# Performance work log

Hardware: AMD Instinct MI355X
Metric: run time of the kernel (lower is better)

The kernel has to match this reference:

```python
import jax, jax.numpy as jnp
import numpy as np

TOPK = 13
NC = 80
ALPHA = 1.0
BETA = 6.0
EPS = 1e-9
TN = 256
IMG = 640


def _make_anchor_points():
    # standard YOLO anchor centers for strides 8,16,32 on a 640x640 image -> 8400 points
    pts = []
    for s in (8, 16, 32):
        n = IMG // s
        xs = (np.arange(n, dtype=np.float32) + 0.5) * s
        gx, gy = np.meshgrid(xs, xs)
        pts.append(np.stack([gx.ravel(), gy.ravel()], axis=-1))
    return jnp.asarray(np.concatenate(pts, axis=0))  # (8400, 2)


def setup_inputs() -> dict:
    key = jax.random.key(0)
    k1, k2, k3, k4, k5, k6 = jax.random.split(key, 6)
    anc_points = _make_anchor_points()
    grids = anc_points.shape[0]
    pd_scores = jax.random.uniform(k1, (TN, grids, NC), dtype=jnp.float32)
    # predicted boxes: valid xyxy around random centers
    pc = jax.random.uniform(k2, (TN, grids, 2), dtype=jnp.float32) * IMG
    pwh = jax.random.uniform(k3, (TN, grids, 2), dtype=jnp.float32) * 64.0 + 4.0
    pd_bboxes = jnp.concatenate([pc - pwh * 0.5, pc + pwh * 0.5], axis=-1)
    gc = jax.random.uniform(k4, (TN, 2), dtype=jnp.float32) * IMG
    gwh = jax.random.uniform(k5, (TN, 2), dtype=jnp.float32) * 160.0 + 16.0
    gt_bboxes = jnp.concatenate([gc - gwh * 0.5, gc + gwh * 0.5], axis=-1)
    gt_labels = jax.random.randint(k6, (TN, 1), 0, NC, dtype=jnp.int32)
    return {"pd_scores": pd_scores, "pd_bboxes": pd_bboxes, "anc_points": anc_points,
            "gt_labels": gt_labels, "gt_bboxes": gt_bboxes}


def _iou(box1, box2):
    # box1: (tn,4) xyxy, box2: (tn,grids,4) xyxy -> (tn,grids)
    b1 = box1[:, None, :]
    x1y1 = jnp.maximum(b1[..., 0:2], box2[..., 0:2])
    x2y2 = jnp.minimum(b1[..., 2:4], box2[..., 2:4])
    overlap = jnp.clip(x2y2 - x1y1, 0).prod(-1)
    area1 = jnp.clip(b1[..., 2:4] - b1[..., 0:2], 0).prod(-1)
    area2 = jnp.clip(box2[..., 2:4] - box2[..., 0:2], 0).prod(-1)
    return overlap / (area1 + area2 - overlap + EPS)


def _candidates_in_gts(xy_centers, gt_bboxes):
    # xy_centers: (grids,2), gt_bboxes: (tn,4) -> (tn,grids) float {0,1}
    lt = xy_centers[None, :, :] - gt_bboxes[:, None, 0:2]   # (tn,grids,2)
    rb = gt_bboxes[:, None, 2:4] - xy_centers[None, :, :]   # (tn,grids,2)
    deltas = jnp.concatenate([lt, rb], axis=-1)             # (tn,grids,4)
    return (deltas.min(axis=-1) > EPS).astype(gt_bboxes.dtype)


def _topk_mask(metrics):
    # metrics: (tn,grids) -> binary mask of per-row top-k entries
    tn, grids = metrics.shape
    _, idxs = jax.lax.top_k(metrics, TOPK)                  # (tn,TOPK)
    rows = jnp.arange(tn)[:, None]
    return jnp.zeros((tn, grids), metrics.dtype).at[rows, idxs].add(1.0)


def reference(pd_scores, pd_bboxes, anc_points, gt_labels, gt_bboxes):
    tn, grids, nc = pd_scores.shape
    gt_lab = gt_labels.astype(jnp.int32)                    # (tn,1)
    # per-target class score at its gt label: (tn,grids)
    idx = jnp.broadcast_to(gt_lab[:, :, None], (tn, grids, 1))
    bbox_scores = jnp.take_along_axis(pd_scores, idx, axis=2).squeeze(-1)
    overlaps = _iou(gt_bboxes, pd_bboxes)                   # (tn,grids)
    align_metric = (bbox_scores ** ALPHA) * (overlaps ** BETA)
    mask_in_gts = _candidates_in_gts(anc_points, gt_bboxes)
    mask_topk = _topk_mask(align_metric * mask_in_gts)
    mask_pos = mask_topk * mask_in_gts                      # (tn,grids)
    # targets
    target_labels = jnp.where(mask_pos == 1, gt_lab, 0).astype(jnp.int32)  # (tn,grids)
    target_bboxes = jnp.where(mask_pos[..., None] == 1, gt_bboxes[:, None, :], 0.0)
    onehot = jax.nn.one_hot(target_labels, NC, dtype=pd_scores.dtype)
    target_scores = jnp.where(mask_pos[..., None] > 0, onehot, 0.0)
    # normalization of scores by aligned metric
    am = align_metric * mask_pos
    pos_align = am.max(axis=-1, keepdims=True)
    pos_overlaps = (overlaps * mask_pos).max(axis=-1, keepdims=True)
    norm = (am * pos_overlaps / (pos_align + EPS))[..., None]
    target_scores = target_scores * norm
    return target_labels, target_bboxes, target_scores, mask_pos.astype(bool)
```

## Files before the change

### kernel.cpp

```cpp
#include <hip/hip_runtime.h>

#define GRIDS 8400
#define TNB   256
#define NCV   80
#define TOPKV 13
#define EPSF  1e-9f

__global__ __launch_bounds__(256) void taa_kernel(
    const float* __restrict__ pd_scores,
    const float* __restrict__ pd_bboxes,
    const float* __restrict__ anc,
    const int*   __restrict__ gt_labels,
    const float* __restrict__ gt_bboxes,
    float* __restrict__ out_labels,
    float* __restrict__ out_bboxes,
    float* __restrict__ out_scores,
    float* __restrict__ out_mask)
{
    __shared__ float smet[GRIDS];
    __shared__ float rv[256];
    __shared__ int   ri[256];
    __shared__ int   sel_idx[TOPKV];
    __shared__ float sel_val[TOPKV];
    __shared__ float sel_am[TOPKV];
    __shared__ float sel_ov[TOPKV];
    __shared__ int   sel_in[TOPKV];

    const int t   = blockIdx.x;
    const int tid = threadIdx.x;

    const float gx1 = gt_bboxes[t*4+0];
    const float gy1 = gt_bboxes[t*4+1];
    const float gx2 = gt_bboxes[t*4+2];
    const float gy2 = gt_bboxes[t*4+3];
    const int   lab = gt_labels[t];
    const float garea = fmaxf(gx2-gx1, 0.f) * fmaxf(gy2-gy1, 0.f);

    const float4* pb = reinterpret_cast<const float4*>(pd_bboxes) + (size_t)t*GRIDS;
    const float*  ps = pd_scores + (size_t)t*GRIDS*NCV + lab;

    for (int g = tid; g < GRIDS; g += 256) {
        float ax = anc[2*g], ay = anc[2*g+1];
        float dmin = fminf(fminf(ax-gx1, ay-gy1), fminf(gx2-ax, gy2-ay));
        float4 p = pb[g];
        float ix1 = fmaxf(gx1, p.x), iy1 = fmaxf(gy1, p.y);
        float ix2 = fminf(gx2, p.z), iy2 = fminf(gy2, p.w);
        float ov  = fmaxf(ix2-ix1, 0.f) * fmaxf(iy2-iy1, 0.f);
        float pa  = fmaxf(p.z-p.x, 0.f) * fmaxf(p.w-p.y, 0.f);
        float iou = ov / (garea + pa - ov + EPSF);
        float sc  = ps[(size_t)g*NCV];
        float i2  = iou*iou;
        float m   = sc * (i2*i2*i2);
        smet[g] = (dmin > EPSF) ? m : 0.f;
    }
    __syncthreads();

    for (int k = 0; k < TOPKV; ++k) {
        float bv = -1.f; int bi = GRIDS;
        for (int g = tid; g < GRIDS; g += 256) {
            float v = smet[g];
            if (v > bv) { bv = v; bi = g; }
        }
        rv[tid] = bv; ri[tid] = bi;
        __syncthreads();
        for (int s = 128; s > 0; s >>= 1) {
            if (tid < s) {
                float v2 = rv[tid+s]; int j2 = ri[tid+s];
                if (v2 > rv[tid] || (v2 == rv[tid] && j2 < ri[tid])) { rv[tid] = v2; ri[tid] = j2; }
            }
            __syncthreads();
        }
        if (tid == 0) {
            int gi = ri[0];
            sel_idx[k] = gi;
            sel_val[k] = rv[0];
            smet[gi] = -1.f;
        }
        __syncthreads();
    }

    if (tid < TOPKV) {
        int g = sel_idx[tid];
        float ax = anc[2*g], ay = anc[2*g+1];
        float dmin = fminf(fminf(ax-gx1, ay-gy1), fminf(gx2-ax, gy2-ay));
        bool ing = dmin > EPSF;
        float4 p = pb[g];
        float ix1 = fmaxf(gx1, p.x), iy1 = fmaxf(gy1, p.y);
        float ix2 = fminf(gx2, p.z), iy2 = fminf(gy2, p.w);
        float ov  = fmaxf(ix2-ix1, 0.f) * fmaxf(iy2-iy1, 0.f);
        float pa  = fmaxf(p.z-p.x, 0.f) * fmaxf(p.w-p.y, 0.f);
        float iou = ov / (garea + pa - ov + EPSF);
        sel_in[tid] = ing ? 1 : 0;
        sel_am[tid] = ing ? sel_val[tid] : 0.f;
        sel_ov[tid] = ing ? iou : 0.f;
    }
    __syncthreads();

    if (tid < TOPKV && sel_in[tid]) {
        float pa = 0.f, po = 0.f;
        for (int k = 0; k < TOPKV; ++k) {
            pa = fmaxf(pa, sel_am[k]);
            po = fmaxf(po, sel_ov[k]);
        }
        float norm = sel_am[tid] * po / (pa + EPSF);
        int g = sel_idx[tid];
        size_t off = (size_t)t*GRIDS + g;
        out_labels[off] = (float)lab;
        out_mask[off]   = 1.0f;
        float4 gb; gb.x = gx1; gb.y = gy1; gb.z = gx2; gb.w = gy2;
        reinterpret_cast<float4*>(out_bboxes)[off] = gb;
        out_scores[off*(size_t)NCV + lab] = norm;
    }
}

extern "C" void kernel_launch(void* const* d_in, const int* in_sizes, int n_in,
                              void* d_out, int out_size, void* d_ws, size_t ws_size,
                              hipStream_t stream)
{
    const float* pd_scores = (const float*)d_in[0];
    const float* pd_bboxes = (const float*)d_in[1];
    const float* anc       = (const float*)d_in[2];
    const int*   gt_labels = (const int*)d_in[3];
    const float* gt_bboxes = (const float*)d_in[4];
    float* out = (float*)d_out;

    hipMemsetAsync(d_out, 0, (size_t)out_size * sizeof(float), stream);

    float* out_labels = out;
    float* out_bboxes = out_labels + (size_t)TNB*GRIDS;
    float* out_scores = out_bboxes + (size_t)TNB*GRIDS*4;
    float* out_mask   = out_scores + (size_t)TNB*GRIDS*NCV;

    taa_kernel<<<TNB, 256, 0, stream>>>(pd_scores, pd_bboxes, anc, gt_labels, gt_bboxes,
                                        out_labels, out_bboxes, out_scores, out_mask);
}
```

Measured before the change: 1.083 ms.

## Fuse output zero-fill into kernel and use wavefront shuffle reductions

Drops the separate hipMemsetAsync over the whole output and has each block write its full slice (labels, mask, bboxes, scores) with float4 stores, driven by a shared-memory bitmap of selected anchors. The per-iteration top-k block reduction is replaced by wave-level shuffle reductions plus a 4-entry cross-wave combine, which cuts barriers. Anchor and gt loads are vectorised. The risk is that the output write (about 690 MB) now comes from only 256 blocks, which may use less bandwidth than memset. There is also integer division per score chunk.

```diff
diff --git a/kernel.cpp b/kernel.cpp
--- a/kernel.cpp
+++ b/kernel.cpp
@@ -1,12 +1,13 @@
 #include <hip/hip_runtime.h>
 
-#define GRIDS 8400
-#define TNB   256
-#define NCV   80
-#define TOPKV 13
-#define EPSF  1e-9f
+#define GRIDS  8400
+#define TNB    256
+#define NCV    80
+#define TOPKV  13
+#define EPSF   1e-9f
+#define NWORDS 263
 
-__global__ __launch_bounds__(256) void taa_kernel(
+__global__ __launch_bounds__(256) void taa_fused(
     const float* __restrict__ pd_scores,
     const float* __restrict__ pd_bboxes,
     const float* __restrict__ anc,
@@ -18,8 +19,9 @@
     float* __restrict__ out_mask)
 {
     __shared__ float smet[GRIDS];
-    __shared__ float rv[256];
-    __shared__ int   ri[256];
+    __shared__ unsigned bitmap[NWORDS];
+    __shared__ float wv[4];
+    __shared__ int   wi[4];
     __shared__ int   sel_idx[TOPKV];
     __shared__ float sel_val[TOPKV];
     __shared__ float sel_am[TOPKV];
@@ -29,18 +31,19 @@
     const int t   = blockIdx.x;
     const int tid = threadIdx.x;
 
-    const float gx1 = gt_bboxes[t*4+0];
-    const float gy1 = gt_bboxes[t*4+1];
-    const float gx2 = gt_bboxes[t*4+2];
-    const float gy2 = gt_bboxes[t*4+3];
+    const float4 gbb = reinterpret_cast<const float4*>(gt_bboxes)[t];
+    const float gx1 = gbb.x, gy1 = gbb.y, gx2 = gbb.z, gy2 = gbb.w;
     const int   lab = gt_labels[t];
     const float garea = fmaxf(gx2-gx1, 0.f) * fmaxf(gy2-gy1, 0.f);
 
-    const float4* pb = reinterpret_cast<const float4*>(pd_bboxes) + (size_t)t*GRIDS;
-    const float*  ps = pd_scores + (size_t)t*GRIDS*NCV + lab;
+    const float4* pb   = reinterpret_cast<const float4*>(pd_bboxes) + (size_t)t*GRIDS;
+    const float2* anc2 = reinterpret_cast<const float2*>(anc);
+    const float*  ps   = pd_scores + (size_t)t*GRIDS*NCV + lab;
 
+    #pragma unroll 4
     for (int g = tid; g < GRIDS; g += 256) {
-        float ax = anc[2*g], ay = anc[2*g+1];
+        float2 a = anc2[g];
+        float ax = a.x, ay = a.y;
         float dmin = fminf(fminf(ax-gx1, ay-gy1), fminf(gx2-ax, gy2-ay));
         float4 p = pb[g];
         float ix1 = fmaxf(gx1, p.x), iy1 = fmaxf(gy1, p.y);
@@ -61,27 +64,31 @@
             float v = smet[g];
             if (v > bv) { bv = v; bi = g; }
         }
-        rv[tid] = bv; ri[tid] = bi;
+        #pragma unroll
+        for (int off = 32; off > 0; off >>= 1) {
+            float v2 = __shfl_down(bv, off);
+            int   i2 = __shfl_down(bi, off);
+            if (v2 > bv || (v2 == bv && i2 < bi)) { bv = v2; bi = i2; }
+        }
+        if ((tid & 63) == 0) { wv[tid >> 6] = bv; wi[tid >> 6] = bi; }
         __syncthreads();
-        for (int s = 128; s > 0; s >>= 1) {
-            if (tid < s) {
-                float v2 = rv[tid+s]; int j2 = ri[tid+s];
-                if (v2 > rv[tid] || (v2 == rv[tid] && j2 < ri[tid])) { rv[tid] = v2; ri[tid] = j2; }
+        if (tid == 0) {
+            float fv = wv[0]; int fi = wi[0];
+            #pragma unroll
+            for (int w = 1; w < 4; ++w) {
+                float v2 = wv[w]; int i2 = wi[w];
+                if (v2 > fv || (v2 == fv && i2 < fi)) { fv = v2; fi = i2; }
             }
-            __syncthreads();
-        }
-        if (tid == 0) {
-            int gi = ri[0];
-            sel_idx[k] = gi;
-            sel_val[k] = rv[0];
-            smet[gi] = -1.f;
+            sel_idx[k] = fi; sel_val[k] = fv;
+            smet[fi] = -1.f;
         }
         __syncthreads();
     }
 
     if (tid < TOPKV) {
         int g = sel_idx[tid];
-        float ax = anc[2*g], ay = anc[2*g+1];
+        float2 a = anc2[g];
+        float ax = a.x, ay = a.y;
         float dmin = fminf(fminf(ax-gx1, ay-gy1), fminf(gx2-ax, gy2-ay));
         bool ing = dmin > EPSF;
         float4 p = pb[g];
@@ -94,22 +101,60 @@
         sel_am[tid] = ing ? sel_val[tid] : 0.f;
         sel_ov[tid] = ing ? iou : 0.f;
     }
+    for (int w = tid; w < NWORDS; w += 256) bitmap[w] = 0u;
     __syncthreads();
 
     if (tid < TOPKV && sel_in[tid]) {
         float pa = 0.f, po = 0.f;
+        #pragma unroll
         for (int k = 0; k < TOPKV; ++k) {
             pa = fmaxf(pa, sel_am[k]);
             po = fmaxf(po, sel_ov[k]);
         }
         float norm = sel_am[tid] * po / (pa + EPSF);
         int g = sel_idx[tid];
-        size_t off = (size_t)t*GRIDS + g;
-        out_labels[off] = (float)lab;
-        out_mask[off]   = 1.0f;
-        float4 gb; gb.x = gx1; gb.y = gy1; gb.z = gx2; gb.w = gy2;
-        reinterpret_cast<float4*>(out_bboxes)[off] = gb;
-        out_scores[off*(size_t)NCV + lab] = norm;
+        smet[g] = norm;
+        atomicOr(&bitmap[g >> 5], 1u << (g & 31));
+    }
+    __syncthreads();
+
+    const float labf = (float)lab;
+    const float4 z4  = {0.f, 0.f, 0.f, 0.f};
+    const float4 gb4 = {gx1, gy1, gx2, gy2};
+    float4* lab4 = reinterpret_cast<float4*>(out_labels + (size_t)t*GRIDS);
+    float4* msk4 = reinterpret_cast<float4*>(out_mask   + (size_t)t*GRIDS);
+    float4* bb4  = reinterpret_cast<float4*>(out_bboxes + (size_t)t*GRIDS*4);
+    float4* sc4  = reinterpret_cast<float4*>(out_scores + (size_t)t*GRIDS*NCV);
+
+    for (int c = tid; c < GRIDS/4; c += 256) {
+        unsigned b = (bitmap[c >> 3] >> ((c & 7) * 4)) & 0xFu;
+        float4 lv = z4, mv = z4;
+        if (b & 1u) { lv.x = labf; mv.x = 1.f; }
+        if (b & 2u) { lv.y = labf; mv.y = 1.f; }
+        if (b & 4u) { lv.z = labf; mv.z = 1.f; }
+        if (b & 8u) { lv.w = labf; mv.w = 1.f; }
+        lab4[c] = lv;
+        msk4[c] = mv;
+    }
+    for (int g = tid; g < GRIDS; g += 256) {
+        bool s = (bitmap[g >> 5] >> (g & 31)) & 1u;
+        bb4[g] = s ? gb4 : z4;
+    }
+    for (int c = tid; c < (GRIDS*NCV)/4; c += 256) {
+        unsigned g = (unsigned)c / 20u;
+        float4 v = z4;
+        if ((bitmap[g >> 5] >> (g & 31)) & 1u) {
+            int cls0 = (c - (int)g*20) * 4;
+            int d = lab - cls0;
+            if ((unsigned)d < 4u) {
+                float nv = smet[g];
+                if (d == 0) v.x = nv;
+                else if (d == 1) v.y = nv;
+                else if (d == 2) v.z = nv;
+                else v.w = nv;
+            }
+        }
+        sc4[c] = v;
     }
 }
 
@@ -124,13 +169,11 @@
     const float* gt_bboxes = (const float*)d_in[4];
     float* out = (float*)d_out;
 
-    hipMemsetAsync(d_out, 0, (size_t)out_size * sizeof(float), stream);
-
     float* out_labels = out;
     float* out_bboxes = out_labels + (size_t)TNB*GRIDS;
     float* out_scores = out_bboxes + (size_t)TNB*GRIDS*4;
     float* out_mask   = out_scores + (size_t)TNB*GRIDS*NCV;
 
-    taa_kernel<<<TNB, 256, 0, stream>>>(pd_scores, pd_bboxes, anc, gt_labels, gt_bboxes,
-                                        out_labels, out_bboxes, out_scores, out_mask);
+    taa_fused<<<TNB, 256, 0, stream>>>(pd_scores, pd_bboxes, anc, gt_labels, gt_bboxes,
+                                       out_labels, out_bboxes, out_scores, out_mask);
 }
```

New measurement: 1.103 ms. No clear change (+1.9%).
